# Kernel tuning notes

Hardware: AMD Instinct MI355X
Metric: run time of the kernel (lower is better)

## Reference

```python
import jax, jax.numpy as jnp
import numpy as np

EPS = 1e-5

def rmsnorm(x, g):
    var = jnp.mean(jnp.square(x), axis=-1, keepdims=True)
    return x * jax.lax.rsqrt(var + EPS) * g

def setup_inputs() -> dict:
    key = jax.random.key(0)
    ks = jax.random.split(key, 8)
    B, S, T, D = 2, 2048, 2048, 1024
    H, HKV, HD = 16, 4, 64
    std = 0.02
    return {
        "x": jax.random.normal(ks[0], (B, S, D), jnp.float32),
        "kv": jax.random.normal(ks[1], (B, T, D), jnp.float32),
        "wq": jax.random.normal(ks[2], (H * HD, D), jnp.float32) * std,
        "wk": jax.random.normal(ks[3], (HKV * HD, D), jnp.float32) * std,
        "wv": jax.random.normal(ks[4], (HKV * HD, D), jnp.float32) * std,
        "wo": jax.random.normal(ks[5], (D, H * HD), jnp.float32) * std,
        "gq": jnp.ones((D,), jnp.float32),
        "gkv": jnp.ones((D,), jnp.float32),
    }

def reference(x, kv, wq, wk, wv, wo, gq, gkv):
    B, S, D = x.shape
    T = kv.shape[1]
    H, HKV, HD = 16, 4, 64
    R = H // HKV  # heads per kv group
    xn = rmsnorm(x, gq)
    kvn = rmsnorm(kv, gkv)
    # projections
    q = (xn @ wq.T).reshape(B, S, HKV, R, HD)   # grouped query heads
    k = (kvn @ wk.T).reshape(B, T, HKV, HD)
    v = (kvn @ wv.T).reshape(B, T, HKV, HD)
    scale = 1.0 / jnp.sqrt(jnp.float32(HD))
    # block-mask is None -> full dense cross attention; GQA via broadcast einsum
    scores = jnp.einsum('bsgrd,btgd->bgrst', q, k) * scale  # [B,HKV,R,S,T]
    probs = jax.nn.softmax(scores, axis=-1)
    out = jnp.einsum('bgrst,btgd->bsgrd', probs, v)  # [B,S,HKV,R,HD]
    out = out.reshape(B, S, H * HD) @ wo.T
    return x + out
```

## Files before the change

### kernel.cpp

```cpp
#include <hip/hip_runtime.h>

#define DEV __device__ __forceinline__

typedef __attribute__((ext_vector_type(8))) _Float16 h8;
typedef __attribute__((ext_vector_type(4))) float f32x4;
typedef __attribute__((ext_vector_type(16))) float f32x16;
typedef __fp16 __attribute__((ext_vector_type(2))) hh2;

DEV unsigned short f2h(float f) {
  union { _Float16 h[2]; unsigned short u[2]; } v;
  v.h[0] = (_Float16)f;
  return v.u[0];
}

DEV void async_load16(const void* g, void* l) {
  __builtin_amdgcn_global_load_lds(
      (const __attribute__((address_space(1))) void*)g,
      (__attribute__((address_space(3))) void*)l,
      16, 0, 0);
}

DEV void pl32swap(unsigned int& a, unsigned int& b) {
  asm("v_permlane32_swap_b32 %0, %1" : "+v"(a), "+v"(b));
}


__global__ __launch_bounds__(256) void prep(const float* __restrict__ x,
                                            const float* __restrict__ kv,
                                            const float* __restrict__ wq,
                                            const float* __restrict__ wk,
                                            const float* __restrict__ wv,
                                            const float* __restrict__ wo,
                                            const float* __restrict__ gq,
                                            const float* __restrict__ gkv,
                                            unsigned short* __restrict__ wqb,
                                            unsigned short* __restrict__ wkvb,
                                            unsigned short* __restrict__ wob,
                                            unsigned short* __restrict__ xn,
                                            unsigned short* __restrict__ kvn,
                                            float qscale) {
  const int b = blockIdx.x, tid = threadIdx.x;
  if (b < 640) {
    const float* src;
    unsigned short* dst;
    float sc = 1.0f;
    int base;
    if (b < 256) { src = wq; dst = wqb; sc = qscale; base = b; }
    else if (b < 320) { src = wk; dst = wkvb; base = b - 256; }
    else if (b < 384) { src = wv; dst = wkvb + 262144; base = b - 320; }
    else { src = wo; dst = wob; base = b - 384; }
#pragma unroll
    for (int j = 0; j < 4; ++j) {
      const int i = base * 4096 + j * 1024 + tid * 4;
      float4 v = *(const float4*)&src[i];
      ushort4 o;
      o.x = f2h(v.x * sc); o.y = f2h(v.y * sc);
      o.z = f2h(v.z * sc); o.w = f2h(v.w * sc);
      *(ushort4*)&dst[i] = o;
    }
    return;
  }
  const int w = tid >> 6, l = tid & 63;
  int row = (b - 640) * 4 + w;
  const float* src;
  const float* g;
  unsigned short* dst;
  if (row < 4096) { src = x; g = gq; dst = xn; }
  else { row -= 4096; src = kv; g = gkv; dst = kvn; }
  const float* xr = src + (size_t)row * 1024;
  float4 v[4];
  float ss = 0.0f;
#pragma unroll
  for (int i = 0; i < 4; ++i) {
    v[i] = *(const float4*)&xr[i * 256 + l * 4];
    ss += v[i].x * v[i].x + v[i].y * v[i].y + v[i].z * v[i].z + v[i].w * v[i].w;
  }
  ss += __shfl_xor(ss, 32); ss += __shfl_xor(ss, 16);
  ss += __shfl_xor(ss, 8);  ss += __shfl_xor(ss, 4);
  ss += __shfl_xor(ss, 2);  ss += __shfl_xor(ss, 1);
  const float inv = rsqrtf(ss * (1.0f / 1024.0f) + 1e-5f);
#pragma unroll
  for (int i = 0; i < 4; ++i) {
    float4 gv = *(const float4*)&g[i * 256 + l * 4];
    ushort4 o;
    o.x = f2h(v[i].x * inv * gv.x); o.y = f2h(v[i].y * inv * gv.y);
    o.z = f2h(v[i].z * inv * gv.z); o.w = f2h(v[i].w * inv * gv.w);
    *(ushort4*)&dst[(size_t)row * 1024 + i * 256 + l * 4] = o;
  }
}

__global__ __launch_bounds__(256, 2) void proj_gemm(const unsigned short* __restrict__ xn,
                                                    const unsigned short* __restrict__ kvn,
                                                    const unsigned short* __restrict__ wqb,
                                                    const unsigned short* __restrict__ wkvb,
                                                    unsigned short* __restrict__ qb,
                                                    unsigned short* __restrict__ kb,
                                                    unsigned short* __restrict__ vTb) {
  __shared__ unsigned short Al[2][2][128 * 32];
  __shared__ unsigned short Bl[2][2][128 * 32];
  const int tid = threadIdx.x;
  const int w = tid >> 6, l = tid & 63;
  const int quad = l >> 4, ln = l & 15;
  const int wm0 = (w >> 1) * 64, wn0 = (w & 1) * 64;
  const int r4 = l >> 2;
  const int c4s = (((l & 3) ^ ((l >> 3) & 3))) * 8;
  const int qs8 = (quad ^ ((l >> 1) & 3)) * 8;

  int z = blockIdx.x;
  const unsigned short *A, *W;
  int m0, n0, isq;
  if (z < 256) {
    A = xn; W = wqb; isq = 1;
    m0 = (((z >> 6) << 3) + (z & 7)) * 128;
    n0 = ((z >> 3) & 7) * 128;
  } else {
    z -= 256; A = kvn; W = wkvb; isq = 0;
    m0 = (((z >> 5) << 3) + (z & 7)) * 128;
    n0 = ((z >> 3) & 3) * 128;
  }

  f32x4 acc[4][4] = {};

  auto stage = [&](int buf, int kk) {
#pragma unroll
    for (int j = 0; j < 8; ++j) {
      const int idx = w * 8 + j;
      if (idx < 16) {
        const int p = idx >> 3, rb = (idx & 7) * 16;
        async_load16(A + (size_t)(m0 + rb + r4) * 1024 + kk + p * 32 + c4s,
                     &Al[buf][p][rb * 32]);
      } else {
        const int ib = idx - 16;
        const int p = ib >> 3, rb = (ib & 7) * 16;
        async_load16(W + (size_t)(n0 + rb + r4) * 1024 + kk + p * 32 + c4s,
                     &Bl[buf][p][rb * 32]);
      }
    }
  };

  stage(0, 0);
  for (int it = 0; it < 16; ++it) {
    const int buf = it & 1;
    __syncthreads();
    if (it < 15) stage(buf ^ 1, (it + 1) * 64);
#pragma unroll
    for (int kc = 0; kc < 2; ++kc) {
      h8 af[4], bf[4];
#pragma unroll
      for (int mi = 0; mi < 4; ++mi)
        af[mi] = *(const h8*)&Al[buf][kc][(wm0 + mi * 16 + ln) * 32 + qs8];
#pragma unroll
      for (int ni = 0; ni < 4; ++ni)
        bf[ni] = *(const h8*)&Bl[buf][kc][(wn0 + ni * 16 + ln) * 32 + qs8];
#pragma unroll
      for (int mi = 0; mi < 4; ++mi)
#pragma unroll
        for (int ni = 0; ni < 4; ++ni)
          acc[mi][ni] = __builtin_amdgcn_mfma_f32_16x16x32_f16(af[mi], bf[ni], acc[mi][ni], 0, 0, 0);
    }
  }

#pragma unroll
  for (int mi = 0; mi < 4; ++mi)
#pragma unroll
    for (int ni = 0; ni < 4; ++ni)
#pragma unroll
      for (int r = 0; r < 4; ++r) {
        const int row = m0 + wm0 + mi * 16 + quad * 4 + r;
        const int col = n0 + wn0 + ni * 16 + ln;
        const unsigned short v = f2h(acc[mi][ni][r]);
        if (isq) {
          qb[((size_t)row << 10) + col] = v;
        } else if (col < 256) {
          kb[(size_t)row * 256 + col] = v;
        } else {
          const int c2 = col - 256, gg = c2 >> 6, dd = c2 & 63;
          const int bb = row >> 11, t = row & 2047;
          vTb[((size_t)((bb * 4 + gg) * 64 + dd) << 11) + t] = v;
        }
      }
}

__global__ __launch_bounds__(256) void o_gemm(const unsigned short* __restrict__ O0,
                                              const unsigned short* __restrict__ O1,
                                              const unsigned short* __restrict__ O2,
                                              const float* __restrict__ l0p,
                                              const float* __restrict__ l1p,
                                              const float* __restrict__ l2p,
                                              const unsigned short* __restrict__ wob,
                                              const float* __restrict__ x,
                                              float* __restrict__ out) {
  __shared__ unsigned short Al[2][2][128 * 32];
  __shared__ unsigned short Bl[2][2][128 * 32];
  __shared__ float Linv[16 * 128];
  const int tid = threadIdx.x;
  const int w = tid >> 6, l = tid & 63;
  const int quad = l >> 4, ln = l & 15;
  const int wm0 = (w >> 1) * 64, wn0 = (w & 1) * 64;
  const int r4 = l >> 2;
  const int c4s = (((l & 3) ^ ((l >> 3) & 3))) * 8;
  const int qs8 = (quad ^ ((l >> 1) & 3)) * 8;

  const int z = blockIdx.x;
  const int m0 = (((z >> 6) << 3) + (z & 7)) * 128;
  const int n0 = ((z >> 3) & 7) * 128;

  {
    const int h = tid >> 4, r0 = (tid & 15) * 8;
#pragma unroll
    for (int i = 0; i < 8; ++i) {
      const int r = r0 + i;
      const size_t li = (size_t)(m0 + r) * 16 + h;
      Linv[h * 128 + r] = 1.0f / (l0p[li] + l1p[li] + l2p[li]);
    }
  }
  __syncthreads();

  const int srow = tid >> 3;
  const int sp = (tid >> 2) & 1;
  const int ss = tid & 3;

  auto stageA = [&](int buf, int kk) {
    const int h = kk >> 6;
#pragma unroll
    for (int ps = 0; ps < 4; ++ps) {
      const int row = ps * 32 + srow;
      const size_t gidx = (size_t)(m0 + row) * 1024 + kk + sp * 32 + ss * 8;
      h8 a0 = *(const h8*)&O0[gidx];
      h8 a1 = *(const h8*)&O1[gidx];
      h8 a2 = *(const h8*)&O2[gidx];
      const _Float16 lv = (_Float16)Linv[h * 128 + row];
      h8 sum = a0 + a1 + a2;
#pragma unroll
      for (int q2 = 0; q2 < 8; ++q2) sum[q2] *= lv;
      const int sl = ss ^ ((row >> 1) & 3);
      *(h8*)&Al[buf][sp][row * 32 + sl * 8] = sum;
    }
  };
  auto stageB = [&](int buf, int kk) {
#pragma unroll
    for (int j = 0; j < 4; ++j) {
      const int ib = w * 4 + j;
      const int p = ib >> 3, rb = (ib & 7) * 16;
      async_load16(wob + (size_t)(n0 + rb + r4) * 1024 + kk + p * 32 + c4s,
                   &Bl[buf][p][rb * 32]);
    }
  };

  f32x4 acc[4][4] = {};
  stageB(0, 0);
  stageA(0, 0);
  for (int it = 0; it < 16; ++it) {
    const int buf = it & 1;
    __syncthreads();
    if (it < 15) { stageB(buf ^ 1, (it + 1) * 64); stageA(buf ^ 1, (it + 1) * 64); }
#pragma unroll
    for (int kc = 0; kc < 2; ++kc) {
      h8 af[4], bf[4];
#pragma unroll
      for (int mi = 0; mi < 4; ++mi)
        af[mi] = *(const h8*)&Al[buf][kc][(wm0 + mi * 16 + ln) * 32 + qs8];
#pragma unroll
      for (int ni = 0; ni < 4; ++ni)
        bf[ni] = *(const h8*)&Bl[buf][kc][(wn0 + ni * 16 + ln) * 32 + qs8];
#pragma unroll
      for (int mi = 0; mi < 4; ++mi)
#pragma unroll
        for (int ni = 0; ni < 4; ++ni)
          acc[mi][ni] = __builtin_amdgcn_mfma_f32_16x16x32_f16(af[mi], bf[ni], acc[mi][ni], 0, 0, 0);
    }
  }

#pragma unroll
  for (int mi = 0; mi < 4; ++mi)
#pragma unroll
    for (int ni = 0; ni < 4; ++ni)
#pragma unroll
      for (int r = 0; r < 4; ++r) {
        const int row = m0 + wm0 + mi * 16 + quad * 4 + r;
        const int col = n0 + wn0 + ni * 16 + ln;
        const size_t idx = ((size_t)row << 10) + col;
        out[idx] = x[idx] + acc[mi][ni][r];
      }
}

__global__ __launch_bounds__(256, 3) void flash_attn(const unsigned short* __restrict__ q,
                                                     const unsigned short* __restrict__ k,
                                                     const unsigned short* __restrict__ vT,
                                                     unsigned short* __restrict__ o0,
                                                     unsigned short* __restrict__ o1,
                                                     unsigned short* __restrict__ o2,
                                                     float* __restrict__ l0p,
                                                     float* __restrict__ l1p,
                                                     float* __restrict__ l2p) {
  __shared__ __align__(16) unsigned short Kl[2][64 * 64];
  __shared__ __align__(16) unsigned short Vl[2][64 * 64];

  const int tid = threadIdx.x;
  const int w = tid >> 6, l = tid & 63;
  const int lq = l & 31, hi = l >> 5;
  const int r8 = l >> 3, c8 = l & 7;
  const int csw = (c8 ^ r8) * 8;
  const int rsw = lq & 7;
  const int s0 = blockIdx.x * 256;
  const int h = blockIdx.y, g = h >> 2;
  const int zz = blockIdx.z;
  const int b = zz / 3, ts = zz - b * 3;
  const int nt = (ts == 2) ? 10 : 11;
  const int tbase = ts * 704;

  unsigned short* Opart = (ts == 0) ? o0 : (ts == 1) ? o1 : o2;
  float* lpart = (ts == 0) ? l0p : (ts == 1) ? l1p : l2p;

  size_t qrow[2];
  qrow[0] = (size_t)(b * 2048 + s0 + w * 64 + lq);
  qrow[1] = qrow[0] + 32;

  h8 qf[2][4];
#pragma unroll
  for (int q2 = 0; q2 < 2; ++q2)
#pragma unroll
    for (int ks = 0; ks < 4; ++ks)
      qf[q2][ks] = *(const h8*)&q[(qrow[q2] << 10) + h * 64 + ks * 16 + hi * 8];

  int aoff[4];
#pragma unroll
  for (int j = 0; j < 4; ++j)
    aoff[j] = (lq * 64 + (((2 * j + hi) ^ rsw)) * 8) * 2;

  f32x16 oacc[2][2] = {};
  float lsum[2] = {0.0f, 0.0f};

  const unsigned short* kbase = k + ((size_t)(b * 2048)) * 256 + g * 64;
  const unsigned short* vbase = vT + (((size_t)(b * 4 + g) * 64) << 11);

  const hh2 one2 = {(__fp16)1.0f, (__fp16)1.0f};

  auto stage = [&](int sb, int t0) {
#pragma unroll
    for (int j = 0; j < 2; ++j) {
      const int idx = w * 2 + j;
      async_load16(kbase + (size_t)(t0 + idx * 8 + r8) * 256 + csw,
                   &Kl[sb][idx * 512]);
      async_load16(vbase + (((size_t)(idx * 8 + r8)) << 11) + t0 + csw,
                   &Vl[sb][idx * 512]);
    }
  };

  stage(0, tbase);
  for (int it = 0; it < nt; ++it) {
    const int buf = it & 1;
    __syncthreads();
    if (it + 1 < nt) stage(buf ^ 1, tbase + (it + 1) * 64);

    const unsigned short* KB = &Kl[buf][0];
    const unsigned short* VB = &Vl[buf][0];

#pragma unroll
    for (int TH = 0; TH < 2; ++TH) {
      h8 kf[4];
#pragma unroll
      for (int ks = 0; ks < 4; ++ks)
        kf[ks] = *(const h8*)((const char*)KB + TH * 4096 + aoff[ks]);
      f32x16 st0 = {}, st1 = {};
      __builtin_amdgcn_s_setprio(1);
#pragma unroll
      for (int ks = 0; ks < 4; ++ks) {
        st0 = __builtin_amdgcn_mfma_f32_32x32x16_f16(kf[ks], qf[0][ks], st0, 0, 0, 0);
        st1 = __builtin_amdgcn_mfma_f32_32x32x16_f16(kf[ks], qf[1][ks], st1, 0, 0, 0);
      }
      __builtin_amdgcn_s_setprio(0);
      unsigned int w0_[8], w1_[8];
#pragma unroll
      for (int j = 0; j < 8; ++j) {
        union { hh2 h2; unsigned int u; } pk0, pk1;
        pk0.h2 = __builtin_amdgcn_cvt_pkrtz(__builtin_amdgcn_exp2f(st0[2 * j]),
                                            __builtin_amdgcn_exp2f(st0[2 * j + 1]));
        pk1.h2 = __builtin_amdgcn_cvt_pkrtz(__builtin_amdgcn_exp2f(st1[2 * j]),
                                            __builtin_amdgcn_exp2f(st1[2 * j + 1]));
        lsum[0] = __builtin_amdgcn_fdot2(pk0.h2, one2, lsum[0], false);
        lsum[1] = __builtin_amdgcn_fdot2(pk1.h2, one2, lsum[1], false);
        w0_[j] = pk0.u; w1_[j] = pk1.u;
      }
      h8 pf0[2], pf1[2];
      {
        unsigned int a0 = w0_[0], b0 = w0_[2]; pl32swap(a0, b0);
        unsigned int a1 = w0_[1], b1 = w0_[3]; pl32swap(a1, b1);
        unsigned int a4 = w0_[4], b4 = w0_[6]; pl32swap(a4, b4);
        unsigned int a5 = w0_[5], b5 = w0_[7]; pl32swap(a5, b5);
        union { unsigned int u[4]; h8 v; } f0, f1;
        f0.u[0] = a0; f0.u[1] = a1; f0.u[2] = b0; f0.u[3] = b1;
        f1.u[0] = a4; f1.u[1] = a5; f1.u[2] = b4; f1.u[3] = b5;
        pf0[0] = f0.v; pf0[1] = f1.v;
        unsigned int c0 = w1_[0], d0 = w1_[2]; pl32swap(c0, d0);
        unsigned int c1 = w1_[1], d1 = w1_[3]; pl32swap(c1, d1);
        unsigned int c4 = w1_[4], d4 = w1_[6]; pl32swap(c4, d4);
        unsigned int c5 = w1_[5], d5 = w1_[7]; pl32swap(c5, d5);
        union { unsigned int u[4]; h8 v; } f2, f3;
        f2.u[0] = c0; f2.u[1] = c1; f2.u[2] = d0; f2.u[3] = d1;
        f3.u[0] = c4; f3.u[1] = c5; f3.u[2] = d4; f3.u[3] = d5;
        pf1[0] = f2.v; pf1[1] = f3.v;
      }
      __builtin_amdgcn_s_setprio(1);
#pragma unroll
      for (int cc = 0; cc < 2; ++cc) {
        const int c = TH * 2 + cc;
        h8 v0 = *(const h8*)((const char*)VB + aoff[c]);
        h8 v1 = *(const h8*)((const char*)VB + 4096 + aoff[c]);
        oacc[0][0] = __builtin_amdgcn_mfma_f32_32x32x16_f16(v0, pf0[cc], oacc[0][0], 0, 0, 0);
        oacc[1][0] = __builtin_amdgcn_mfma_f32_32x32x16_f16(v0, pf1[cc], oacc[1][0], 0, 0, 0);
        oacc[0][1] = __builtin_amdgcn_mfma_f32_32x32x16_f16(v1, pf0[cc], oacc[0][1], 0, 0, 0);
        oacc[1][1] = __builtin_amdgcn_mfma_f32_32x32x16_f16(v1, pf1[cc], oacc[1][1], 0, 0, 0);
      }
      __builtin_amdgcn_s_setprio(0);
    }
  }

#pragma unroll
  for (int q2 = 0; q2 < 2; ++q2) {
    float ls = lsum[q2];
    ls += __shfl_xor(ls, 32);
    if (l < 32) lpart[qrow[q2] * 16 + h] = ls;
#pragma unroll
    for (int dblk = 0; dblk < 2; ++dblk)
#pragma unroll
      for (int qd = 0; qd < 4; ++qd) {
        ushort4 o;
        o.x = f2h(oacc[q2][dblk][qd * 4 + 0]);
        o.y = f2h(oacc[q2][dblk][qd * 4 + 1]);
        o.z = f2h(oacc[q2][dblk][qd * 4 + 2]);
        o.w = f2h(oacc[q2][dblk][qd * 4 + 3]);
        *(ushort4*)&Opart[(qrow[q2] << 10) + h * 64 + dblk * 32 + qd * 8 + hi * 4] = o;
      }
  }
}

extern "C" void kernel_launch(void* const* d_in, const int* in_sizes, int n_in,
                              void* d_out, int out_size, void* d_ws, size_t ws_size,
                              hipStream_t stream) {
  const float* x   = (const float*)d_in[0];
  const float* kv  = (const float*)d_in[1];
  const float* wq  = (const float*)d_in[2];
  const float* wk  = (const float*)d_in[3];
  const float* wv  = (const float*)d_in[4];
  const float* wo  = (const float*)d_in[5];
  const float* gq  = (const float*)d_in[6];
  const float* gkv = (const float*)d_in[7];

  char* ws = (char*)d_ws;
  unsigned short* xn   = (unsigned short*)(ws);
  unsigned short* kvn  = (unsigned short*)(ws + 8388608);
  unsigned short* qb   = (unsigned short*)(ws + 16777216);
  unsigned short* kb   = (unsigned short*)(ws + 25165824);
  unsigned short* vTb  = (unsigned short*)(ws + 27262976);
  unsigned short* O2   = (unsigned short*)(ws + 29360128);
  unsigned short* wqb  = (unsigned short*)(ws + 37748736);
  unsigned short* wkvb = (unsigned short*)(ws + 39845888);
  unsigned short* wob  = (unsigned short*)(ws + 40894464);
  unsigned short* Opart0 = xn;
  unsigned short* Opart1 = kvn;
  float* l0p = (float*)wqb;
  float* l1p = (float*)(ws + 37748736 + 262144);
  float* l2p = (float*)(ws + 37748736 + 524288);

  const float qscale = 0.18033688011112042f;

  prep<<<2688, 256, 0, stream>>>(x, kv, wq, wk, wv, wo, gq, gkv,
                                 wqb, wkvb, wob, xn, kvn, qscale);

  proj_gemm<<<384, 256, 0, stream>>>(xn, kvn, wqb, wkvb, qb, kb, vTb);

  flash_attn<<<dim3(8, 16, 6), 256, 0, stream>>>(qb, kb, vTb, Opart0, Opart1, O2,
                                                 l0p, l1p, l2p);

  o_gemm<<<256, 256, 0, stream>>>(Opart0, Opart1, O2, l0p, l1p, l2p, wob, x, (float*)d_out);
}
```

Baseline: 198.4 us.

## Use 128-wide KV tiles and a two-way KV split in flash attention

The flash attention kernel now splits the KV sequence into two halves instead of three, so the grid shrinks from 768 to 512 blocks. Each iteration stages 128 keys and values instead of 64, which halves the number of barrier and stage iterations. Occupancy drops to two blocks per CU because LDS doubles and the launch bound changes. The output GEMM now reduces only two partial outputs and row sums, which saves one partial-buffer read. The fewer, larger blocks risk a worse fill of the available CUs.

```diff
diff --git a/kernel.cpp b/kernel.cpp
--- a/kernel.cpp
+++ b/kernel.cpp
@@ -183,10 +183,8 @@
 
 __global__ __launch_bounds__(256) void o_gemm(const unsigned short* __restrict__ O0,
                                               const unsigned short* __restrict__ O1,
-                                              const unsigned short* __restrict__ O2,
                                               const float* __restrict__ l0p,
                                               const float* __restrict__ l1p,
-                                              const float* __restrict__ l2p,
                                               const unsigned short* __restrict__ wob,
                                               const float* __restrict__ x,
                                               float* __restrict__ out) {
@@ -211,7 +209,7 @@
     for (int i = 0; i < 8; ++i) {
       const int r = r0 + i;
       const size_t li = (size_t)(m0 + r) * 16 + h;
-      Linv[h * 128 + r] = 1.0f / (l0p[li] + l1p[li] + l2p[li]);
+      Linv[h * 128 + r] = 1.0f / (l0p[li] + l1p[li]);
     }
   }
   __syncthreads();
@@ -228,9 +226,8 @@
       const size_t gidx = (size_t)(m0 + row) * 1024 + kk + sp * 32 + ss * 8;
       h8 a0 = *(const h8*)&O0[gidx];
       h8 a1 = *(const h8*)&O1[gidx];
-      h8 a2 = *(const h8*)&O2[gidx];
       const _Float16 lv = (_Float16)Linv[h * 128 + row];
-      h8 sum = a0 + a1 + a2;
+      h8 sum = a0 + a1;
 #pragma unroll
       for (int q2 = 0; q2 < 8; ++q2) sum[q2] *= lv;
       const int sl = ss ^ ((row >> 1) & 3);
@@ -284,33 +281,30 @@
       }
 }
 
-__global__ __launch_bounds__(256, 3) void flash_attn(const unsigned short* __restrict__ q,
+__global__ __launch_bounds__(256, 2) void flash_attn(const unsigned short* __restrict__ q,
                                                      const unsigned short* __restrict__ k,
                                                      const unsigned short* __restrict__ vT,
                                                      unsigned short* __restrict__ o0,
                                                      unsigned short* __restrict__ o1,
-                                                     unsigned short* __restrict__ o2,
                                                      float* __restrict__ l0p,
-                                                     float* __restrict__ l1p,
-                                                     float* __restrict__ l2p) {
-  __shared__ __align__(16) unsigned short Kl[2][64 * 64];
-  __shared__ __align__(16) unsigned short Vl[2][64 * 64];
+                                                     float* __restrict__ l1p) {
+  __shared__ __align__(16) unsigned short Kl[2][128 * 64];
+  __shared__ __align__(16) unsigned short Vl[2][64 * 128];
 
   const int tid = threadIdx.x;
   const int w = tid >> 6, l = tid & 63;
   const int lq = l & 31, hi = l >> 5;
   const int r8 = l >> 3, c8 = l & 7;
+  const int c16 = l & 15, r16v = l >> 4;
   const int csw = (c8 ^ r8) * 8;
   const int rsw = lq & 7;
   const int s0 = blockIdx.x * 256;
   const int h = blockIdx.y, g = h >> 2;
-  const int zz = blockIdx.z;
-  const int b = zz / 3, ts = zz - b * 3;
-  const int nt = (ts == 2) ? 10 : 11;
-  const int tbase = ts * 704;
-
-  unsigned short* Opart = (ts == 0) ? o0 : (ts == 1) ? o1 : o2;
-  float* lpart = (ts == 0) ? l0p : (ts == 1) ? l1p : l2p;
+  const int b = blockIdx.z >> 1, ts = blockIdx.z & 1;
+  const int tbase = ts << 10;
+
+  unsigned short* Opart = ts ? o1 : o0;
+  float* lpart = ts ? l1p : l0p;
 
   size_t qrow[2];
   qrow[0] = (size_t)(b * 2048 + s0 + w * 64 + lq);
@@ -327,6 +321,10 @@
 #pragma unroll
   for (int j = 0; j < 4; ++j)
     aoff[j] = (lq * 64 + (((2 * j + hi) ^ rsw)) * 8) * 2;
+  int voff[8];
+#pragma unroll
+  for (int j = 0; j < 8; ++j)
+    voff[j] = (lq * 128 + (((2 * j + hi) ^ rsw)) * 8) * 2;
 
   f32x16 oacc[2][2] = {};
   float lsum[2] = {0.0f, 0.0f};
@@ -338,26 +336,27 @@
 
   auto stage = [&](int sb, int t0) {
 #pragma unroll
-    for (int j = 0; j < 2; ++j) {
-      const int idx = w * 2 + j;
+    for (int j = 0; j < 4; ++j) {
+      const int idx = w * 4 + j;
       async_load16(kbase + (size_t)(t0 + idx * 8 + r8) * 256 + csw,
                    &Kl[sb][idx * 512]);
-      async_load16(vbase + (((size_t)(idx * 8 + r8)) << 11) + t0 + csw,
+      const int vrow = idx * 4 + r16v;
+      async_load16(vbase + (((size_t)vrow) << 11) + t0 + ((c16 ^ (vrow & 7)) * 8),
                    &Vl[sb][idx * 512]);
     }
   };
 
   stage(0, tbase);
-  for (int it = 0; it < nt; ++it) {
+  for (int it = 0; it < 8; ++it) {
     const int buf = it & 1;
     __syncthreads();
-    if (it + 1 < nt) stage(buf ^ 1, tbase + (it + 1) * 64);
+    if (it < 7) stage(buf ^ 1, tbase + (it + 1) * 128);
 
     const unsigned short* KB = &Kl[buf][0];
     const unsigned short* VB = &Vl[buf][0];
 
 #pragma unroll
-    for (int TH = 0; TH < 2; ++TH) {
+    for (int TH = 0; TH < 4; ++TH) {
       h8 kf[4];
 #pragma unroll
       for (int ks = 0; ks < 4; ++ks)
@@ -405,8 +404,8 @@
 #pragma unroll
       for (int cc = 0; cc < 2; ++cc) {
         const int c = TH * 2 + cc;
-        h8 v0 = *(const h8*)((const char*)VB + aoff[c]);
-        h8 v1 = *(const h8*)((const char*)VB + 4096 + aoff[c]);
+        h8 v0 = *(const h8*)((const char*)VB + voff[c]);
+        h8 v1 = *(const h8*)((const char*)VB + 8192 + voff[c]);
         oacc[0][0] = __builtin_amdgcn_mfma_f32_32x32x16_f16(v0, pf0[cc], oacc[0][0], 0, 0, 0);
         oacc[1][0] = __builtin_amdgcn_mfma_f32_32x32x16_f16(v0, pf1[cc], oacc[1][0], 0, 0, 0);
         oacc[0][1] = __builtin_amdgcn_mfma_f32_32x32x16_f16(v1, pf0[cc], oacc[0][1], 0, 0, 0);
@@ -453,7 +452,6 @@
   unsigned short* qb   = (unsigned short*)(ws + 16777216);
   unsigned short* kb   = (unsigned short*)(ws + 25165824);
   unsigned short* vTb  = (unsigned short*)(ws + 27262976);
-  unsigned short* O2   = (unsigned short*)(ws + 29360128);
   unsigned short* wqb  = (unsigned short*)(ws + 37748736);
   unsigned short* wkvb = (unsigned short*)(ws + 39845888);
   unsigned short* wob  = (unsigned short*)(ws + 40894464);
@@ -461,7 +459,6 @@
   unsigned short* Opart1 = kvn;
   float* l0p = (float*)wqb;
   float* l1p = (float*)(ws + 37748736 + 262144);
-  float* l2p = (float*)(ws + 37748736 + 524288);
 
   const float qscale = 0.18033688011112042f;
 
@@ -470,8 +467,7 @@
 
   proj_gemm<<<384, 256, 0, stream>>>(xn, kvn, wqb, wkvb, qb, kb, vTb);
 
-  flash_attn<<<dim3(8, 16, 6), 256, 0, stream>>>(qb, kb, vTb, Opart0, Opart1, O2,
-                                                 l0p, l1p, l2p);
-
-  o_gemm<<<256, 256, 0, stream>>>(Opart0, Opart1, O2, l0p, l1p, l2p, wob, x, (float*)d_out);
-}
+  flash_attn<<<dim3(8, 16, 4), 256, 0, stream>>>(qb, kb, vTb, Opart0, Opart1, l0p, l1p);
+
+  o_gemm<<<256, 256, 0, stream>>>(Opart0, Opart1, l0p, l1p, wob, x, (float*)d_out);
+}
```

After: 191.7 us. 3.4% less time.
